# Optimization experiments

Hardware: AMD Instinct MI355X
Metric: run time of the kernel (lower is better)

Reference implementation:

```python
import jax, jax.numpy as jnp
import numpy as np

N_HEADS = 8
D_MODEL = 256
HEAD_DEPTH = D_MODEL // N_HEADS
B, S = 2, 4096


def setup_inputs() -> dict:
    key = jax.random.key(0)
    ks = jax.random.split(key, 8)
    scale = 1.0 / np.sqrt(D_MODEL)
    return {
        "q": jax.random.normal(ks[0], (B, S, D_MODEL), dtype=jnp.float32),
        "k": jax.random.normal(ks[1], (B, S, D_MODEL), dtype=jnp.float32),
        "v": jax.random.normal(ks[2], (B, S, D_MODEL), dtype=jnp.float32),
        "mask": jax.random.randint(ks[3], (B, S, S), 0, 2).astype(jnp.bool_),
        "wq": jax.random.normal(ks[4], (D_MODEL, D_MODEL), dtype=jnp.float32) * scale,
        "wk": jax.random.normal(ks[5], (D_MODEL, D_MODEL), dtype=jnp.float32) * scale,
        "wv": jax.random.normal(ks[6], (D_MODEL, D_MODEL), dtype=jnp.float32) * scale,
        "w_out": jax.random.normal(ks[7], (D_MODEL, D_MODEL), dtype=jnp.float32) * scale,
    }


def _split_heads(x):
    # [B, S, D] -> [B, H, S, Dh]
    b, s, _ = x.shape
    return x.reshape(b, s, N_HEADS, HEAD_DEPTH).transpose(0, 2, 1, 3)


def reference(q, k, v, mask, wq, wk, wv, w_out):
    Q = _split_heads(q @ wq)
    K = _split_heads(k @ wk)
    V = _split_heads(v @ wv)
    # [B, H, Sq, Sk]
    scores = jnp.einsum('bhqd,bhkd->bhqk', Q, K) / jnp.sqrt(
        jnp.asarray(HEAD_DEPTH, dtype=Q.dtype))
    # mask True -> -inf, broadcast over heads
    scores = jnp.where(mask[:, None, :, :], -jnp.inf, scores)
    probs = jax.nn.softmax(scores, axis=-1)
    attn = jnp.einsum('bhqk,bhkd->bhqd', probs, V)
    attn = attn.transpose(0, 2, 1, 3).reshape(q.shape[0], -1, D_MODEL)
    return attn @ w_out
```

## Files before the change

### kernel.cpp

```cpp
#include <hip/hip_runtime.h>
#include <stdint.h>

typedef __bf16 bf16;
typedef __bf16 bf16x8 __attribute__((ext_vector_type(8)));
typedef __bf16 bf16x4 __attribute__((ext_vector_type(4)));
typedef float  f32x4  __attribute__((ext_vector_type(4)));
typedef float  f32x8  __attribute__((ext_vector_type(8)));
typedef float  f32x16 __attribute__((ext_vector_type(16)));
typedef float  float4v __attribute__((ext_vector_type(4)));
typedef int    int4v   __attribute__((ext_vector_type(4)));
typedef unsigned int uint;
typedef unsigned long long ull;

#define QSCALE 0.25505003984214403f


__global__ __launch_bounds__(256) void transpose_w(
    const float* __restrict__ w0, const float* __restrict__ w1,
    const float* __restrict__ w2, const float* __restrict__ w3,
    bf16* __restrict__ WT) {
  const int wsel = blockIdx.z;
  const float* W = wsel == 0 ? w0 : wsel == 1 ? w1 : wsel == 2 ? w2 : w3;
  const int k0 = blockIdx.x * 64, n0 = blockIdx.y * 64;
  __shared__ __align__(16) bf16 t[64][72];
  const int tid = threadIdx.x;
  {
    const int kk = (tid >> 4) << 2;
    const int nn = (tid & 15) << 2;
#pragma unroll
    for (int r = 0; r < 4; ++r) {
      float4v a = *(const float4v*)(W + (size_t)(k0 + kk + r) * 256 + n0 + nn);
#pragma unroll
      for (int j = 0; j < 4; ++j) t[nn + j][kk + r] = (bf16)a[j];
    }
  }
  __syncthreads();
  {
    const int ni = tid >> 2;
    const int c  = (tid & 3) * 16;
    bf16x8 o0 = *(const bf16x8*)(&t[ni][c]);
    bf16x8 o1 = *(const bf16x8*)(&t[ni][c + 8]);
    bf16* dst = WT + (size_t)wsel * 65536 + (size_t)(n0 + ni) * 256 + k0 + c;
    *(bf16x8*)dst = o0;
    *(bf16x8*)(dst + 8) = o1;
  }
}

__global__ __launch_bounds__(256) void proj_pack(
    const float* __restrict__ xq, const float* __restrict__ xk, const float* __restrict__ xv,
    const bf16* __restrict__ WT,
    bf16* __restrict__ Qp, bf16* __restrict__ Kp, bf16* __restrict__ Vp,
    const int* __restrict__ mask, uint* __restrict__ M2) {
  __shared__ __align__(16) unsigned char smem[18432];
  const int tid = threadIdx.x;

  if (blockIdx.x >= 768) {
    uint* trans = (uint*)smem;
    const int pid = blockIdx.x - 768;
    const int bb = pid >> 8;
    const int qt = (pid >> 2) & 63, kc = pid & 3;
    const int q0 = qt * 64;
    const int w = tid >> 6, l = tid & 63;
    const int qrow = q0 + w * 16 + (l >> 2);
    const size_t rowbase = ((size_t)(bb * 4096 + qrow)) * 4096 + kc * 1024;
#pragma unroll
    for (int p = 0; p < 8; ++p) {
      const int kdw = p * 4 + (l & 3);
      const int4v* mp = (const int4v*)(mask + rowbase + kdw * 32);
      uint bits = 0;
#pragma unroll
      for (int j = 0; j < 8; ++j) {
        int4v m = mp[j];
#pragma unroll
        for (int i = 0; i < 4; ++i) bits |= (m[i] != 0 ? 1u : 0u) << (j * 4 + i);
      }
      trans[kdw * 72 + w * 16 + (l >> 2)] = bits;
    }
    __syncthreads();
    {
      const int r = tid >> 3, c = (tid & 7) * 4;
      int4v a = *(const int4v*)(trans + r * 72 + c);
      int4v d = *(const int4v*)(trans + r * 72 + c + 32);
      uint* o = M2 + ((size_t)(bb * 128 + kc * 32 + r)) * 4096 + q0;
      *(int4v*)(o + c) = a;
      *(int4v*)(o + c + 32) = d;
    }
    return;
  }

  const int z = blockIdx.x >> 8;
  const int r8 = blockIdx.x & 255;
  const int m0 = (r8 >> 1) * 64, n0 = (r8 & 1) * 128;
  const float* X = z == 0 ? xq : (z == 1 ? xk : xv);
  const bf16* wt = WT + (size_t)z * 65536;
  const int wave = tid >> 6, lane = tid & 63;
  const int nl = lane & 15, quad = lane >> 4;
  const int arow = m0 + wave * 16 + nl;
  const float* xrow = X + (size_t)arow * 256;

  f32x4 zero4 = {0.f, 0.f, 0.f, 0.f};
  f32x4 acc[8];
#pragma unroll
  for (int i = 0; i < 8; ++i) acc[i] = zero4;

  for (int ks = 0; ks < 8; ++ks) {
    float4v a0 = *(const float4v*)(xrow + ks * 32 + quad * 8);
    float4v a1 = *(const float4v*)(xrow + ks * 32 + quad * 8 + 4);
    bf16x8 af;
#pragma unroll
    for (int i = 0; i < 4; ++i) { af[i] = (bf16)a0[i]; af[4 + i] = (bf16)a1[i]; }
#pragma unroll
    for (int nf = 0; nf < 8; ++nf) {
      bf16x8 bfr = *(const bf16x8*)(wt + (size_t)(n0 + nf * 16 + nl) * 256 + ks * 32 + quad * 8);
      acc[nf] = __builtin_amdgcn_mfma_f32_16x16x32_bf16(af, bfr, acc[nf], 0, 0, 0);
    }
  }

  const int bq = m0 >> 12;
  const int s0 = m0 & 4095;
  const int posl = wave * 16 + quad * 4;

  if (z == 2) {
    bf16* tv = (bf16*)smem;
#pragma unroll
    for (int nf = 0; nf < 8; ++nf) {
      const int col = nf * 16 + nl;
      bf16x4 o;
#pragma unroll
      for (int rr = 0; rr < 4; ++rr) o[rr] = (bf16)acc[nf][rr];
      *(bf16x4*)(tv + (size_t)col * 72 + posl) = o;
    }
    __syncthreads();
    const int h2 = tid >> 6, ln = tid & 63;
    const int d = ln & 31, shalf = ln >> 5;
    const int h = (n0 >> 5) + h2;
    bf16* vb = Vp + (size_t)(bq * 8 + h) * 131072 + (size_t)(s0 >> 5) * 1024 + d * 8;
#pragma unroll
    for (int it = 0; it < 4; ++it) {
      const int blk = it >> 1, sub = (it & 1) * 2 + shalf;
      const int K0 = (sub >> 1) * 16 + (sub & 1) * 4;
      const bf16* src = tv + (size_t)(h2 * 32 + d) * 72 + blk * 32 + K0;
      bf16x4 g0 = *(const bf16x4*)(src);
      bf16x4 g1 = *(const bf16x4*)(src + 8);
      bf16x8 o;
#pragma unroll
      for (int j = 0; j < 4; ++j) { o[j] = g0[j]; o[4 + j] = g1[j]; }
      *(bf16x8*)(vb + (size_t)blk * 1024 + sub * 256) = o;
    }
  } else {
    bf16* tq = (bf16*)smem;
    const float scale = (z == 0) ? QSCALE : 1.0f;
#pragma unroll
    for (int nf = 0; nf < 8; ++nf) {
      const int col = nf * 16 + nl;
#pragma unroll
      for (int rr = 0; rr < 4; ++rr)
        tq[(size_t)(posl + rr) * 136 + col] = (bf16)(acc[nf][rr] * scale);
    }
    __syncthreads();
    bf16* Out = z == 0 ? Qp : Kp;
    const int h2 = tid >> 6, ln = tid & 63;
    const int h = (n0 >> 5) + h2;
    const int s = s0 + ln;
    bf16* ob = Out + (size_t)(bq * 8 + h) * 131072 + (size_t)(s >> 5) * 1024 + (s & 31) * 8;
#pragma unroll
    for (int sub = 0; sub < 4; ++sub) {
      bf16x8 o = *(const bf16x8*)(tq + (size_t)ln * 136 + h2 * 32 + sub * 8);
      *(bf16x8*)(ob + sub * 256) = o;
    }
  }
}

__global__ __launch_bounds__(256) void attn_kernel(
    const bf16* __restrict__ Qp, const bf16* __restrict__ Kp,
    const bf16* __restrict__ Vp, const uint* __restrict__ M2,
    bf16* __restrict__ Og) {
  const int id = blockIdx.x;
  const int xcd = id & 7, slot = id >> 3;
  const int bh = xcd * 2 + (slot >> 6);
  const int q0 = (slot & 63) * 64;
  const int b = bh >> 3, h = bh & 7;
  const int tid = threadIdx.x, w = tid >> 6, lane = tid & 63;
  const int nl = lane & 31, half = lane >> 5;

  __shared__ float Ored[4][32][66];
  __shared__ float Lsum[64][8];

  const size_t bhbase = (size_t)bh * 131072;
  const int so0 = half * 256 + nl * 8;
  const int so1 = 512 + half * 256 + nl * 8;

  bf16x8 qf[2][2];
#pragma unroll
  for (int qt = 0; qt < 2; ++qt) {
    const bf16* qb = Qp + bhbase + (size_t)((q0 >> 5) + qt) * 1024;
    qf[qt][0] = *(const bf16x8*)(qb + so0);
    qf[qt][1] = *(const bf16x8*)(qb + so1);
  }

  const bf16* Kw = Kp + bhbase + (size_t)w * 1024;
  const bf16* Vw = Vp + bhbase + (size_t)w * 1024;
  const uint* Mw = M2 + (size_t)b * 524288 + (size_t)w * 4096 + q0 + nl;

  f32x16 z16;
#pragma unroll
  for (int i = 0; i < 16; ++i) z16[i] = 0.f;
  f32x16 acc0 = z16, acc1 = z16;
  f32x4 ls0 = {0.f, 0.f, 0.f, 0.f}, ls1 = {0.f, 0.f, 0.f, 0.f};

  struct Frag { bf16x8 ka0, ka1, va0, va1; uint m0, m1; };
  auto LOADF = [&](int kt) -> Frag {
    Frag f;
    const bf16* kc = Kw + (size_t)kt * 4096;
    const bf16* vc = Vw + (size_t)kt * 4096;
    f.ka0 = *(const bf16x8*)(kc + so0);
    f.ka1 = *(const bf16x8*)(kc + so1);
    f.va0 = *(const bf16x8*)(vc + so0);
    f.va1 = *(const bf16x8*)(vc + so1);
    const uint* mp = Mw + (size_t)kt * 16384;
    f.m0 = mp[0];
    f.m1 = mp[32];
    return f;
  };

  auto STEP = [&](const Frag& f) {
    const int minv0 = (int)((~f.m0) >> (4 * half));
    const int minv1 = (int)((~f.m1) >> (4 * half));
    __builtin_amdgcn_s_setprio(1);
    f32x16 st0 = __builtin_amdgcn_mfma_f32_32x32x16_bf16(f.ka0, qf[0][0], z16, 0, 0, 0);
    st0 = __builtin_amdgcn_mfma_f32_32x32x16_bf16(f.ka1, qf[0][1], st0, 0, 0, 0);
    f32x16 st1 = __builtin_amdgcn_mfma_f32_32x32x16_bf16(f.ka0, qf[1][0], z16, 0, 0, 0);
    st1 = __builtin_amdgcn_mfma_f32_32x32x16_bf16(f.ka1, qf[1][1], st1, 0, 0, 0);
    __builtin_amdgcn_s_setprio(0);

    f32x16 pf0, pf1;
#pragma unroll
    for (int g = 0; g < 4; ++g)
#pragma unroll
      for (int r = 0; r < 4; ++r) {
        const int i = g * 4 + r, off = r + 8 * g;
        float e0 = __builtin_amdgcn_exp2f(st0[i]);
        float e1 = __builtin_amdgcn_exp2f(st1[i]);
        const uint k0m = (uint)__builtin_amdgcn_sbfe(minv0, off, 1);
        const uint k1m = (uint)__builtin_amdgcn_sbfe(minv1, off, 1);
        e0 = __uint_as_float(__float_as_uint(e0) & k0m);
        e1 = __uint_as_float(__float_as_uint(e1) & k1m);
        ls0[g] += e0; ls1[g] += e1;
        pf0[i] = e0; pf1[i] = e1;
      }
    const bf16x8 pb00 = __builtin_convertvector(
        __builtin_shufflevector(pf0, pf0, 0, 1, 2, 3, 4, 5, 6, 7), bf16x8);
    const bf16x8 pb01 = __builtin_convertvector(
        __builtin_shufflevector(pf0, pf0, 8, 9, 10, 11, 12, 13, 14, 15), bf16x8);
    const bf16x8 pb10 = __builtin_convertvector(
        __builtin_shufflevector(pf1, pf1, 0, 1, 2, 3, 4, 5, 6, 7), bf16x8);
    const bf16x8 pb11 = __builtin_convertvector(
        __builtin_shufflevector(pf1, pf1, 8, 9, 10, 11, 12, 13, 14, 15), bf16x8);

    __builtin_amdgcn_s_setprio(1);
    acc0 = __builtin_amdgcn_mfma_f32_32x32x16_bf16(f.va0, pb00, acc0, 0, 0, 0);
    acc0 = __builtin_amdgcn_mfma_f32_32x32x16_bf16(f.va1, pb01, acc0, 0, 0, 0);
    acc1 = __builtin_amdgcn_mfma_f32_32x32x16_bf16(f.va0, pb10, acc1, 0, 0, 0);
    acc1 = __builtin_amdgcn_mfma_f32_32x32x16_bf16(f.va1, pb11, acc1, 0, 0, 0);
    __builtin_amdgcn_s_setprio(0);
  };

  Frag fa = LOADF(0), fb;
  for (int kt = 0; kt < 32; kt += 2) {
    fb = LOADF(kt + 1);
    STEP(fa);
    if (kt + 2 < 32) fa = LOADF(kt + 2);
    STEP(fb);
  }
  const float lsum0 = (ls0[0] + ls0[1]) + (ls0[2] + ls0[3]);
  const float lsum1 = (ls1[0] + ls1[1]) + (ls1[2] + ls1[3]);

#pragma unroll
  for (int g = 0; g < 4; ++g)
#pragma unroll
    for (int r = 0; r < 4; ++r) {
      const int d = r + 8 * g + 4 * half, i = g * 4 + r;
      Ored[w][d][nl] = acc0[i];
      Ored[w][d][32 + nl] = acc1[i];
    }
  Lsum[nl][w * 2 + half] = lsum0;
  Lsum[32 + nl][w * 2 + half] = lsum1;
  __syncthreads();
  if (tid < 64) {
    float s = 0.f;
#pragma unroll
    for (int j = 0; j < 8; ++j) s += Lsum[tid][j];
    Lsum[tid][0] = 1.0f / s;
  }
  __syncthreads();
  {
    const int q = tid >> 2, db = (tid & 3) * 8;
    const float rl = Lsum[q][0];
    bf16x8 o;
#pragma unroll
    for (int dj = 0; dj < 8; ++dj) {
      const float s = Ored[0][db + dj][q] + Ored[1][db + dj][q] +
                      Ored[2][db + dj][q] + Ored[3][db + dj][q];
      o[dj] = (bf16)(s * rl);
    }
    *(bf16x8*)(Og + ((size_t)(b * 4096 + q0 + q)) * 256 + h * 32 + db) = o;
  }
}

__global__ __launch_bounds__(256) void gemm_out(
    const bf16* __restrict__ A, const bf16* __restrict__ WTo, float* __restrict__ C) {
  const int m0 = blockIdx.x * 64, n0 = blockIdx.y * 64;
  const int tid = threadIdx.x, wave = tid >> 6, lane = tid & 63;
  const int nl = lane & 15, quad = lane >> 4;
  const int arow = m0 + wave * 16 + nl;

  f32x4 zero4 = {0.f, 0.f, 0.f, 0.f};
  f32x4 acc[4];
#pragma unroll
  for (int i = 0; i < 4; ++i) acc[i] = zero4;

  for (int ks = 0; ks < 8; ++ks) {
    bf16x8 af = *(const bf16x8*)(A + (size_t)arow * 256 + ks * 32 + quad * 8);
#pragma unroll
    for (int nf = 0; nf < 4; ++nf) {
      bf16x8 bfr = *(const bf16x8*)(WTo + (size_t)(n0 + nf * 16 + nl) * 256 + ks * 32 + quad * 8);
      acc[nf] = __builtin_amdgcn_mfma_f32_16x16x32_bf16(af, bfr, acc[nf], 0, 0, 0);
    }
  }
  const int Rbase = m0 + wave * 16 + quad * 4;
#pragma unroll
  for (int nf = 0; nf < 4; ++nf)
#pragma unroll
    for (int r = 0; r < 4; ++r)
      C[(size_t)(Rbase + r) * 256 + n0 + nf * 16 + nl] = acc[nf][r];
}

extern "C" void kernel_launch(void* const* d_in, const int* in_sizes, int n_in,
                              void* d_out, int out_size, void* d_ws, size_t ws_size,
                              hipStream_t stream) {
  const float* q  = (const float*)d_in[0];
  const float* k  = (const float*)d_in[1];
  const float* v  = (const float*)d_in[2];
  const int*  mask = (const int*)d_in[3];
  const float* wq = (const float*)d_in[4];
  const float* wk = (const float*)d_in[5];
  const float* wv = (const float*)d_in[6];
  const float* wo = (const float*)d_in[7];
  float* out = (float*)d_out;

  uint8_t* ws = (uint8_t*)d_ws;
  bf16* WT = (bf16*)ws;
  bf16* Qp = (bf16*)(ws + (512u << 10));
  bf16* Kp = Qp + 2097152;
  bf16* Vp = Kp + 2097152;
  uint* Mb = (uint*)((uint8_t*)(Vp + 2097152));
  bf16* Ao = (bf16*)((uint8_t*)Mb + (4u << 20));

  transpose_w<<<dim3(4, 4, 4), 256, 0, stream>>>(wq, wk, wv, wo, WT);
  proj_pack<<<dim3(768 + 512), 256, 0, stream>>>(q, k, v, WT, Qp, Kp, Vp, mask, Mb);
  attn_kernel<<<dim3(1024), 256, 0, stream>>>(Qp, Kp, Vp, Mb, Ao);
  gemm_out<<<dim3(128, 4), 256, 0, stream>>>(Ao, WT + 3 * 65536, out);
}
```

Before: 334.2 us.

## Halve attention query tile, fold mask as -inf bias, compute row sums via MFMA

```diff
diff --git a/kernel.cpp b/kernel.cpp
--- a/kernel.cpp
+++ b/kernel.cpp
@@ -177,38 +177,39 @@
     bf16* __restrict__ Og) {
   const int id = blockIdx.x;
   const int xcd = id & 7, slot = id >> 3;
-  const int bh = xcd * 2 + (slot >> 6);
-  const int q0 = (slot & 63) * 64;
+  const int bh = xcd * 2 + (slot >> 7);
+  const int q0 = (slot & 127) * 32;
   const int b = bh >> 3, h = bh & 7;
   const int tid = threadIdx.x, w = tid >> 6, lane = tid & 63;
   const int nl = lane & 31, half = lane >> 5;
 
-  __shared__ float Ored[4][32][66];
-  __shared__ float Lsum[64][8];
+  __shared__ float Ored[4][32][33];
+  __shared__ float Lsum[32][4];
 
   const size_t bhbase = (size_t)bh * 131072;
   const int so0 = half * 256 + nl * 8;
   const int so1 = 512 + half * 256 + nl * 8;
 
-  bf16x8 qf[2][2];
-#pragma unroll
-  for (int qt = 0; qt < 2; ++qt) {
-    const bf16* qb = Qp + bhbase + (size_t)((q0 >> 5) + qt) * 1024;
-    qf[qt][0] = *(const bf16x8*)(qb + so0);
-    qf[qt][1] = *(const bf16x8*)(qb + so1);
+  bf16x8 qf0, qf1;
+  {
+    const bf16* qb = Qp + bhbase + (size_t)(q0 >> 5) * 1024;
+    qf0 = *(const bf16x8*)(qb + so0);
+    qf1 = *(const bf16x8*)(qb + so1);
   }
 
   const bf16* Kw = Kp + bhbase + (size_t)w * 1024;
   const bf16* Vw = Vp + bhbase + (size_t)w * 1024;
   const uint* Mw = M2 + (size_t)b * 524288 + (size_t)w * 4096 + q0 + nl;
 
-  f32x16 z16;
-#pragma unroll
-  for (int i = 0; i < 16; ++i) z16[i] = 0.f;
-  f32x16 acc0 = z16, acc1 = z16;
-  f32x4 ls0 = {0.f, 0.f, 0.f, 0.f}, ls1 = {0.f, 0.f, 0.f, 0.f};
-
-  struct Frag { bf16x8 ka0, ka1, va0, va1; uint m0, m1; };
+  f32x16 acc, lacc;
+#pragma unroll
+  for (int i = 0; i < 16; ++i) { acc[i] = 0.f; lacc[i] = 0.f; }
+
+  bf16x8 ones;
+#pragma unroll
+  for (int i = 0; i < 8; ++i) ones[i] = (bf16)1.0f;
+
+  struct Frag { bf16x8 ka0, ka1, va0, va1; uint m0; };
   auto LOADF = [&](int kt) -> Frag {
     Frag f;
     const bf16* kc = Kw + (size_t)kt * 4096;
@@ -217,51 +218,40 @@
     f.ka1 = *(const bf16x8*)(kc + so1);
     f.va0 = *(const bf16x8*)(vc + so0);
     f.va1 = *(const bf16x8*)(vc + so1);
-    const uint* mp = Mw + (size_t)kt * 16384;
-    f.m0 = mp[0];
-    f.m1 = mp[32];
+    f.m0 = Mw[(size_t)kt * 16384];
     return f;
   };
 
   auto STEP = [&](const Frag& f) {
-    const int minv0 = (int)((~f.m0) >> (4 * half));
-    const int minv1 = (int)((~f.m1) >> (4 * half));
-    __builtin_amdgcn_s_setprio(1);
-    f32x16 st0 = __builtin_amdgcn_mfma_f32_32x32x16_bf16(f.ka0, qf[0][0], z16, 0, 0, 0);
-    st0 = __builtin_amdgcn_mfma_f32_32x32x16_bf16(f.ka1, qf[0][1], st0, 0, 0, 0);
-    f32x16 st1 = __builtin_amdgcn_mfma_f32_32x32x16_bf16(f.ka0, qf[1][0], z16, 0, 0, 0);
-    st1 = __builtin_amdgcn_mfma_f32_32x32x16_bf16(f.ka1, qf[1][1], st1, 0, 0, 0);
-    __builtin_amdgcn_s_setprio(0);
-
-    f32x16 pf0, pf1;
+    const int mpos = (int)(f.m0 >> (4 * half));
+    f32x16 bias;
 #pragma unroll
     for (int g = 0; g < 4; ++g)
 #pragma unroll
       for (int r = 0; r < 4; ++r) {
         const int i = g * 4 + r, off = r + 8 * g;
-        float e0 = __builtin_amdgcn_exp2f(st0[i]);
-        float e1 = __builtin_amdgcn_exp2f(st1[i]);
-        const uint k0m = (uint)__builtin_amdgcn_sbfe(minv0, off, 1);
-        const uint k1m = (uint)__builtin_amdgcn_sbfe(minv1, off, 1);
-        e0 = __uint_as_float(__float_as_uint(e0) & k0m);
-        e1 = __uint_as_float(__float_as_uint(e1) & k1m);
-        ls0[g] += e0; ls1[g] += e1;
-        pf0[i] = e0; pf1[i] = e1;
+        const uint mb = (uint)__builtin_amdgcn_sbfe(mpos, off, 1);
+        bias[i] = __uint_as_float(mb & 0xFF800000u);
       }
-    const bf16x8 pb00 = __builtin_convertvector(
-        __builtin_shufflevector(pf0, pf0, 0, 1, 2, 3, 4, 5, 6, 7), bf16x8);
-    const bf16x8 pb01 = __builtin_convertvector(
-        __builtin_shufflevector(pf0, pf0, 8, 9, 10, 11, 12, 13, 14, 15), bf16x8);
-    const bf16x8 pb10 = __builtin_convertvector(
-        __builtin_shufflevector(pf1, pf1, 0, 1, 2, 3, 4, 5, 6, 7), bf16x8);
-    const bf16x8 pb11 = __builtin_convertvector(
-        __builtin_shufflevector(pf1, pf1, 8, 9, 10, 11, 12, 13, 14, 15), bf16x8);
-
     __builtin_amdgcn_s_setprio(1);
-    acc0 = __builtin_amdgcn_mfma_f32_32x32x16_bf16(f.va0, pb00, acc0, 0, 0, 0);
-    acc0 = __builtin_amdgcn_mfma_f32_32x32x16_bf16(f.va1, pb01, acc0, 0, 0, 0);
-    acc1 = __builtin_amdgcn_mfma_f32_32x32x16_bf16(f.va0, pb10, acc1, 0, 0, 0);
-    acc1 = __builtin_amdgcn_mfma_f32_32x32x16_bf16(f.va1, pb11, acc1, 0, 0, 0);
+    f32x16 st = __builtin_amdgcn_mfma_f32_32x32x16_bf16(f.ka0, qf0, bias, 0, 0, 0);
+    st = __builtin_amdgcn_mfma_f32_32x32x16_bf16(f.ka1, qf1, st, 0, 0, 0);
+    __builtin_amdgcn_s_setprio(0);
+
+    f32x16 pf;
+#pragma unroll
+    for (int i = 0; i < 16; ++i) pf[i] = __builtin_amdgcn_exp2f(st[i]);
+
+    const bf16x8 pb0 = __builtin_convertvector(
+        __builtin_shufflevector(pf, pf, 0, 1, 2, 3, 4, 5, 6, 7), bf16x8);
+    const bf16x8 pb1 = __builtin_convertvector(
+        __builtin_shufflevector(pf, pf, 8, 9, 10, 11, 12, 13, 14, 15), bf16x8);
+
+    __builtin_amdgcn_s_setprio(1);
+    acc  = __builtin_amdgcn_mfma_f32_32x32x16_bf16(f.va0, pb0, acc, 0, 0, 0);
+    acc  = __builtin_amdgcn_mfma_f32_32x32x16_bf16(f.va1, pb1, acc, 0, 0, 0);
+    lacc = __builtin_amdgcn_mfma_f32_32x32x16_bf16(ones, pb0, lacc, 0, 0, 0);
+    lacc = __builtin_amdgcn_mfma_f32_32x32x16_bf16(ones, pb1, lacc, 0, 0, 0);
     __builtin_amdgcn_s_setprio(0);
   };
 
@@ -272,38 +262,28 @@
     if (kt + 2 < 32) fa = LOADF(kt + 2);
     STEP(fb);
   }
-  const float lsum0 = (ls0[0] + ls0[1]) + (ls0[2] + ls0[3]);
-  const float lsum1 = (ls1[0] + ls1[1]) + (ls1[2] + ls1[3]);
 
 #pragma unroll
   for (int g = 0; g < 4; ++g)
 #pragma unroll
     for (int r = 0; r < 4; ++r) {
       const int d = r + 8 * g + 4 * half, i = g * 4 + r;
-      Ored[w][d][nl] = acc0[i];
-      Ored[w][d][32 + nl] = acc1[i];
-    }
-  Lsum[nl][w * 2 + half] = lsum0;
-  Lsum[32 + nl][w * 2 + half] = lsum1;
-  __syncthreads();
-  if (tid < 64) {
-    float s = 0.f;
-#pragma unroll
-    for (int j = 0; j < 8; ++j) s += Lsum[tid][j];
-    Lsum[tid][0] = 1.0f / s;
-  }
+      Ored[w][d][nl] = acc[i];
+    }
+  if (half == 0) Lsum[nl][w] = lacc[0];
   __syncthreads();
   {
-    const int q = tid >> 2, db = (tid & 3) * 8;
-    const float rl = Lsum[q][0];
-    bf16x8 o;
-#pragma unroll
-    for (int dj = 0; dj < 8; ++dj) {
-      const float s = Ored[0][db + dj][q] + Ored[1][db + dj][q] +
-                      Ored[2][db + dj][q] + Ored[3][db + dj][q];
-      o[dj] = (bf16)(s * rl);
-    }
-    *(bf16x8*)(Og + ((size_t)(b * 4096 + q0 + q)) * 256 + h * 32 + db) = o;
+    const int q = tid >> 3, d0 = (tid & 7) * 4;
+    const float s = Lsum[q][0] + Lsum[q][1] + Lsum[q][2] + Lsum[q][3];
+    const float rl = 1.0f / s;
+    bf16x4 o;
+#pragma unroll
+    for (int dj = 0; dj < 4; ++dj) {
+      const int d = d0 + dj;
+      const float sum = Ored[0][d][q] + Ored[1][d][q] + Ored[2][d][q] + Ored[3][d][q];
+      o[dj] = (bf16)(sum * rl);
+    }
+    *(bf16x4*)(Og + ((size_t)(b * 4096 + q0 + q)) * 256 + h * 32 + d0) = o;
   }
 }
 
@@ -358,6 +338,6 @@
 
   transpose_w<<<dim3(4, 4, 4), 256, 0, stream>>>(wq, wk, wv, wo, WT);
   proj_pack<<<dim3(768 + 512), 256, 0, stream>>>(q, k, v, WT, Qp, Kp, Vp, mask, Mb);
-  attn_kernel<<<dim3(1024), 256, 0, stream>>>(Qp, Kp, Vp, Mb, Ao);
+  attn_kernel<<<dim3(2048), 256, 0, stream>>>(Qp, Kp, Vp, Mb, Ao);
   gemm_out<<<dim3(128, 4), 256, 0, stream>>>(Ao, WT + 3 * 65536, out);
 }
```

New measurement: 328.6 us. Within noise of the previous version (-1.7%).
